# Kernel tuning notes

Hardware: AMD Instinct MI355X
Metric: run time of the kernel (lower is better)

The kernel has to match this reference:

```python
import jax, jax.numpy as jnp
import numpy as np

N_NODES = 100000
NEG_SLOPE = 0.2


def glorot(key, shape):
    fan_in, fan_out = shape[0], shape[-1]
    lim = jnp.sqrt(6.0 / (fan_in + fan_out))
    return jax.random.uniform(key, shape, jnp.float32, -lim, lim)


def setup_inputs() -> dict:
    key = jax.random.key(0)
    ks = jax.random.split(key, 16)
    x = jax.random.normal(ks[0], (N_NODES, 128), jnp.float32)
    edge_index = jax.random.randint(ks[1], (2, 1600000), 0, N_NODES, jnp.int64)
    H1, C1 = 4, 32
    C2 = 64
    return {
        "x": x,
        "edge_index": edge_index,
        # layer 1: GATv2Conv(128 -> 32, heads=4, concat)
        "Wl1": glorot(ks[2], (128, H1 * C1)), "bl1": jnp.zeros((H1 * C1,), jnp.float32),
        "Wr1": glorot(ks[3], (128, H1 * C1)), "br1": jnp.zeros((H1 * C1,), jnp.float32),
        "att1": glorot(ks[4], (H1, C1)),
        "bias1": jnp.zeros((H1 * C1,), jnp.float32),
        # layer 2: GATv2Conv(128 -> 64, heads=1, concat)
        "Wl2": glorot(ks[5], (H1 * C1, C2)), "bl2": jnp.zeros((C2,), jnp.float32),
        "Wr2": glorot(ks[6], (H1 * C1, C2)), "br2": jnp.zeros((C2,), jnp.float32),
        "att2": glorot(ks[7], (1, C2)),
        "bias2": jnp.zeros((C2,), jnp.float32),
    }


def gatv2_layer(x, src, dst, Wl, bl, Wr, br, att, bias):
    # x: [N, F_in]; src/dst: [E] (self-loops already appended)
    H, C = att.shape
    n = x.shape[0]
    xl = (x @ Wl + bl).reshape(n, H, C)  # source transform
    xr = (x @ Wr + br).reshape(n, H, C)  # target transform
    e = jax.nn.leaky_relu(xl[src] + xr[dst], NEG_SLOPE)          # [E, H, C]
    score = jnp.einsum('ehc,hc->eh', e, att)                     # [E, H]
    # segment softmax over incoming edges of each destination node
    smax = jax.ops.segment_max(score, dst, num_segments=n)       # [N, H]
    ex = jnp.exp(score - smax[dst])
    denom = jax.ops.segment_sum(ex, dst, num_segments=n)
    alpha = ex / denom[dst]                                      # [E, H]
    out = jax.ops.segment_sum(alpha[:, :, None] * xl[src], dst, num_segments=n)
    return out.reshape(n, H * C) + bias


def reference(x, edge_index, Wl1, bl1, Wr1, br1, att1, bias1,
              Wl2, bl2, Wr2, br2, att2, bias2):
    n = x.shape[0]
    loops = jnp.arange(n, dtype=edge_index.dtype)
    src = jnp.concatenate([edge_index[0], loops])
    dst = jnp.concatenate([edge_index[1], loops])
    h = gatv2_layer(x, src, dst, Wl1, bl1, Wr1, br1, att1, bias1)
    h = jax.nn.relu(h)
    out = gatv2_layer(h, src, dst, Wl2, bl2, Wr2, br2, att2, bias2)
    return out
```

## Files before the change

### kernel.cpp

```cpp
#include <hip/hip_runtime.h>
#include <hip/hip_fp16.h>

#define NEG 0.2f

typedef _Float16 f16x8 __attribute__((ext_vector_type(8)));
typedef _Float16 f16x2 __attribute__((ext_vector_type(2)));
typedef float    f32x4 __attribute__((ext_vector_type(4)));

__device__ __forceinline__ float fdot2h(__half2 a, __half2 b, float c) {
    return __builtin_amdgcn_fdot2(__builtin_bit_cast(f16x2, a),
                                  __builtin_bit_cast(f16x2, b), c, false);
}

__device__ __forceinline__ __half2 u2h2(unsigned int u) {
    return __builtin_bit_cast(__half2, u);
}

__device__ __forceinline__ __half2 hmax2(__half2 a, __half2 b) {
    unsigned int ua = __builtin_bit_cast(unsigned int, a);
    unsigned int ub = __builtin_bit_cast(unsigned int, b);
    unsigned int ud;
    asm("v_pk_max_f16 %0, %1, %2" : "=v"(ud) : "v"(ua), "v"(ub));
    return __builtin_bit_cast(__half2, ud);
}

template<int CTRL>
__device__ __forceinline__ float dppadd(float x) {
    int xi = __builtin_bit_cast(int, x);
    int yi = __builtin_amdgcn_update_dpp(0, xi, CTRL, 0xf, 0xf, true);
    return x + __builtin_bit_cast(float, yi);
}

template<int CPW, bool IN_F16, bool HPL>
__global__ __launch_bounds__(256) void mfma_gemm_k(
    const float* __restrict__ Xf, const __half* __restrict__ Xh,
    const float* __restrict__ Wl, const float* __restrict__ bl,
    const float* __restrict__ Wr, const float* __restrict__ br,
    __half* __restrict__ YL, __half* __restrict__ YR, int nrows)
{
    __shared__ _Float16 Xs[128 * 136];
    __shared__ _Float16 Ws[128 * 136];

    const int t    = threadIdx.x;
    const int row0 = blockIdx.x * 128;
    const int c0   = blockIdx.y * 128;

    if constexpr (IN_F16) {
        for (int i = t; i < 128 * 16; i += 256) {
            int r = i >> 4, c = i & 15;
            int gr = row0 + r;
            uint4 v = make_uint4(0u, 0u, 0u, 0u);
            if (gr < nrows) v = ((const uint4*)Xh)[(long)gr * 16 + c];
            *(uint4*)&Xs[r * 136 + c * 8] = v;
        }
    } else {
        for (int i = t; i < 128 * 16; i += 256) {
            int r = i >> 4, c = i & 15;
            int gr = row0 + r;
            float4 a = make_float4(0.f,0.f,0.f,0.f), b4 = make_float4(0.f,0.f,0.f,0.f);
            if (gr < nrows) {
                a  = ((const float4*)Xf)[(long)gr * 32 + c * 2];
                b4 = ((const float4*)Xf)[(long)gr * 32 + c * 2 + 1];
            }
            _Float16 h[8] = {(_Float16)a.x,(_Float16)a.y,(_Float16)a.z,(_Float16)a.w,
                             (_Float16)b4.x,(_Float16)b4.y,(_Float16)b4.z,(_Float16)b4.w};
            *(f16x8*)&Xs[r * 136 + c * 8] = *(f16x8*)h;
        }
    }

    for (int i = t; i < 128 * 128; i += 256) {
        int k = i >> 7, n = i & 127;
        int gc = c0 + n;
        const float* Wp = (gc >= CPW) ? Wr : Wl;
        int lc = gc & (CPW - 1);
        Ws[n * 136 + k] = (_Float16)Wp[(long)k * CPW + lc];
    }
    __syncthreads();

    const int lane  = t & 63;
    const int wv    = t >> 6;
    const int m     = lane & 15;
    const int quad  = lane >> 4;
    const int rbase = wv * 32;

    f16x8 Af[2][4];
    #pragma unroll
    for (int rt = 0; rt < 2; ++rt)
        #pragma unroll
        for (int ks = 0; ks < 4; ++ks)
            Af[rt][ks] = *(const f16x8*)&Xs[(rbase + rt * 16 + m) * 136 + ks * 32 + quad * 8];

    f32x4 acc[2][8];
    #pragma unroll
    for (int rt = 0; rt < 2; ++rt)
        #pragma unroll
        for (int ct = 0; ct < 8; ++ct)
            acc[rt][ct] = (f32x4){0.f, 0.f, 0.f, 0.f};

    #pragma unroll
    for (int ct = 0; ct < 8; ++ct) {
        #pragma unroll
        for (int ks = 0; ks < 4; ++ks) {
            f16x8 Bf = *(const f16x8*)&Ws[(ct * 16 + m) * 136 + ks * 32 + quad * 8];
            acc[0][ct] = __builtin_amdgcn_mfma_f32_16x16x32_f16(Af[0][ks], Bf, acc[0][ct], 0, 0, 0);
            acc[1][ct] = __builtin_amdgcn_mfma_f32_16x16x32_f16(Af[1][ks], Bf, acc[1][ct], 0, 0, 0);
        }
    }

    #pragma unroll
    for (int ct = 0; ct < 8; ++ct) {
        int gc = c0 + ct * 16 + m;
        int which = gc / CPW;
        int lc = gc % CPW;
        _Float16* Y = (_Float16*)(which ? YR : YL);
        float bv = (which ? br : bl)[lc];
        #pragma unroll
        for (int rt = 0; rt < 2; ++rt) {
            int rr = row0 + rbase + rt * 16 + quad * 4;
            #pragma unroll
            for (int g = 0; g < 4; ++g) {
                int r = rr + g;
                if (r < nrows) {
                    long idx;
                    if (HPL && which == 0)
                        idx = (long)(lc >> 6) * ((long)nrows * 64) + (long)r * 64 + (lc & 63);
                    else
                        idx = (long)r * CPW + lc;
                    Y[idx] = (_Float16)(acc[rt][ct][g] + bv);
                }
            }
        }
    }
}


__global__ __launch_bounds__(256) void h1_k(
    const int* __restrict__ ei, int* __restrict__ gh, int E0, int ET, int NBK)
{
    __shared__ int h[256];
    const int t = threadIdx.x, blk = blockIdx.x;
    h[t] = 0;
    __syncthreads();
    int e = blk * 4096 + t;
    #pragma unroll
    for (int u = 0; u < 16; ++u, e += 256) {
        if (e < ET) {
            int dst = (e < E0) ? ei[E0 + e] : (e - E0);
            atomicAdd(&h[dst >> 9], 1);
        }
    }
    __syncthreads();
    gh[t * NBK + blk] = h[t];
}

__global__ __launch_bounds__(256) void scan1_k(
    const int* __restrict__ cnt, int* __restrict__ loc, int* __restrict__ bsum, int n)
{
    __shared__ int wsum[4];
    int t = threadIdx.x;
    int i0 = blockIdx.x * 1024 + t * 4;
    int4 v;
    v.x = (i0 + 0 < n) ? cnt[i0 + 0] : 0;
    v.y = (i0 + 1 < n) ? cnt[i0 + 1] : 0;
    v.z = (i0 + 2 < n) ? cnt[i0 + 2] : 0;
    v.w = (i0 + 3 < n) ? cnt[i0 + 3] : 0;
    int tsum = v.x + v.y + v.z + v.w;
    int incl = tsum;
    #pragma unroll
    for (int s = 1; s < 64; s <<= 1) {
        int u = __shfl_up(incl, s, 64);
        if ((t & 63) >= s) incl += u;
    }
    int wid = t >> 6;
    if ((t & 63) == 63) wsum[wid] = incl;
    __syncthreads();
    int woff = 0;
    #pragma unroll
    for (int w = 0; w < 4; ++w) if (w < wid) woff += wsum[w];
    int ex = woff + incl - tsum;
    if (i0 + 0 < n) loc[i0 + 0] = ex;
    if (i0 + 1 < n) loc[i0 + 1] = ex + v.x;
    if (i0 + 2 < n) loc[i0 + 2] = ex + v.x + v.y;
    if (i0 + 3 < n) loc[i0 + 3] = ex + v.x + v.y + v.z;
    if (t == 255) bsum[blockIdx.x] = woff + incl;
}

__global__ void scan2_k(const int* __restrict__ bsum, int* __restrict__ bcarry,
                        int M, int* __restrict__ total_out)
{
    int lane = threadIdx.x;
    int carry = 0;
    for (int base = 0; base < M; base += 64) {
        int i = base + lane;
        int v = (i < M) ? bsum[i] : 0;
        int incl = v;
        #pragma unroll
        for (int s = 1; s < 64; s <<= 1) {
            int u = __shfl_up(incl, s, 64);
            if (lane >= s) incl += u;
        }
        if (i < M) bcarry[i] = carry + incl - v;
        carry += __shfl(incl, 63, 64);
    }
    if (lane == 0) *total_out = carry;
}

__global__ __launch_bounds__(256) void scan3_k(
    int* __restrict__ off, const int* __restrict__ bcarry, int n)
{
    int i = blockIdx.x * 256 + threadIdx.x;
    if (i >= n) return;
    off[i] += bcarry[i >> 10];
}

__global__ __launch_bounds__(256) void sc1_k(
    const int* __restrict__ ei, const int* __restrict__ gh,
    uint2* __restrict__ rec, int E0, int ET, int NBK)
{
    __shared__ int lofs[256];
    const int t = threadIdx.x, blk = blockIdx.x;
    lofs[t] = gh[t * NBK + blk];
    __syncthreads();
    int e = blk * 4096 + t;
    #pragma unroll
    for (int u = 0; u < 16; ++u, e += 256) {
        if (e < ET) {
            int src = (e < E0) ? ei[e]      : (e - E0);
            int dst = (e < E0) ? ei[E0 + e] : (e - E0);
            int p = atomicAdd(&lofs[dst >> 9], 1);
            rec[p] = make_uint2((unsigned)src, (unsigned)dst);
        }
    }
}

__global__ __launch_bounds__(256) void p2_k(
    const uint2* __restrict__ rec, const int* __restrict__ gh,
    int* __restrict__ srcs, int* __restrict__ off, int N, int NBK)
{
    __shared__ int hist[512];
    __shared__ int sc[2][512];
    __shared__ int curo[512];
    const int t = threadIdx.x;
    const int b = blockIdx.x;
    const int base = gh[b * NBK];
    const int end  = gh[(b + 1) * NBK];
    hist[t] = 0; hist[t + 256] = 0;
    __syncthreads();
    for (int i = base + t; i < end; i += 256) {
        uint2 r = rec[i];
        atomicAdd(&hist[r.y & 511], 1);
    }
    __syncthreads();
    sc[0][t] = hist[t]; sc[0][t + 256] = hist[t + 256];
    __syncthreads();
    int pp = 0;
    for (int s = 1; s < 512; s <<= 1, pp ^= 1) {
        int j0 = t, j1 = t + 256;
        sc[pp ^ 1][j0] = sc[pp][j0] + ((j0 >= s) ? sc[pp][j0 - s] : 0);
        sc[pp ^ 1][j1] = sc[pp][j1] + ((j1 >= s) ? sc[pp][j1 - s] : 0);
        __syncthreads();
    }
    {
        int j0 = t, j1 = t + 256;
        int e0 = base + sc[pp][j0] - hist[j0];
        int e1 = base + sc[pp][j1] - hist[j1];
        curo[j0] = e0;
        curo[j1] = e1;
        int d0 = b * 512 + j0, d1 = b * 512 + j1;
        if (d0 < N) off[d0] = e0;
        if (d1 < N) off[d1] = e1;
    }
    __syncthreads();
    for (int i = base + t; i < end; i += 256) {
        uint2 r = rec[i];
        int pos = atomicAdd(&curo[r.y & 511], 1);
        srcs[pos] = (int)r.x;
    }
}

template<bool RELU>
__global__ __launch_bounds__(256) void fused128hp_k(
    const __half* __restrict__ XLp, const __half* __restrict__ XR,
    const float* __restrict__ ATT, const int* __restrict__ srcs,
    const int* __restrict__ off, const float* __restrict__ bias,
    __half* __restrict__ OUT, int N, int p)
{
    const int t   = threadIdx.x;
    const int d   = blockIdx.x * 32 + (t >> 3);
    const int sub = t & 7;
    const bool nv = d < N;

    int a = 0, b = 0;
    if (nv) { a = off[d]; b = off[d + 1]; }

    __half2 xr[4] = { u2h2(0), u2h2(0), u2h2(0), u2h2(0) };
    if (nv) {
        uint4 ur = *(const uint4*)(XR + (long)d * 128 + p * 64 + sub * 8);
        xr[0] = u2h2(ur.x); xr[1] = u2h2(ur.y); xr[2] = u2h2(ur.z); xr[3] = u2h2(ur.w);
    }
    float4 at0f = ((const float4*)ATT)[p * 16 + sub * 2];
    float4 at1f = ((const float4*)ATT)[p * 16 + sub * 2 + 1];
    __half2 at[4] = { __floats2half2_rn(at0f.x, at0f.y), __floats2half2_rn(at0f.z, at0f.w),
                      __floats2half2_rn(at1f.x, at1f.y), __floats2half2_rn(at1f.z, at1f.w) };
    const __half2 neg2 = __float2half2_rn(NEG);

    float l = 0.f;
    float accv[8] = {0.f,0.f,0.f,0.f,0.f,0.f,0.f,0.f};

    const uint4* XL4 = (const uint4*)(XLp + (size_t)p * N * 64);

    if (b > a) {
        const int bm1 = b - 1;
        int sA = srcs[a];
        uint4 r0 = XL4[(long)sA * 8 + sub];
        int i1 = (a + 1 < bm1) ? a + 1 : bm1;
        int sB = srcs[i1];
        uint4 r1 = XL4[(long)sB * 8 + sub];
        int i2 = (a + 2 < bm1) ? a + 2 : bm1;
        int s2 = srcs[i2];

        for (int e = a; e < b; ++e) {
            uint4 r2 = XL4[(long)s2 * 8 + sub];
            int i3 = (e + 3 < bm1) ? e + 3 : bm1;
            int s3 = srcs[i3];

            __half2 x0 = u2h2(r0.x), x1 = u2h2(r0.y), x2 = u2h2(r0.z), x3 = u2h2(r0.w);
            __half2 s0h = __hadd2(x0, xr[0]);
            __half2 s1h = __hadd2(x1, xr[1]);
            __half2 s2h = __hadd2(x2, xr[2]);
            __half2 s3h = __hadd2(x3, xr[3]);
            __half2 q0 = hmax2(s0h, __hmul2(s0h, neg2));
            __half2 q1 = hmax2(s1h, __hmul2(s1h, neg2));
            __half2 q2 = hmax2(s2h, __hmul2(s2h, neg2));
            __half2 q3 = hmax2(s3h, __hmul2(s3h, neg2));
            float p0 = fdot2h(q0, at[0], 0.f);
            p0 = fdot2h(q1, at[1], p0);
            p0 = fdot2h(q2, at[2], p0);
            p0 = fdot2h(q3, at[3], p0);
            p0 = dppadd<0xB1>(p0);
            p0 = dppadd<0x4E>(p0);
            float ex = __expf(p0);
            l += ex;
            float2 f0 = __half22float2(x0), f1 = __half22float2(x1);
            float2 f2 = __half22float2(x2), f3 = __half22float2(x3);
            accv[0] += ex * f0.x; accv[1] += ex * f0.y;
            accv[2] += ex * f1.x; accv[3] += ex * f1.y;
            accv[4] += ex * f2.x; accv[5] += ex * f2.y;
            accv[6] += ex * f3.x; accv[7] += ex * f3.y;

            r0 = r1; r1 = r2; s2 = s3;
        }
    }

    if (nv) {
        float inv = 1.f / l;
        float4 b0 = ((const float4*)bias)[p * 16 + sub * 2];
        float4 b1 = ((const float4*)bias)[p * 16 + sub * 2 + 1];
        float o[8] = { accv[0]*inv + b0.x, accv[1]*inv + b0.y,
                       accv[2]*inv + b0.z, accv[3]*inv + b0.w,
                       accv[4]*inv + b1.x, accv[5]*inv + b1.y,
                       accv[6]*inv + b1.z, accv[7]*inv + b1.w };
        if constexpr (RELU) {
            #pragma unroll
            for (int j = 0; j < 8; ++j) o[j] = fmaxf(o[j], 0.f);
        }
        uint4 uo;
        uo.x = __builtin_bit_cast(unsigned int, __floats2half2_rn(o[0], o[1]));
        uo.y = __builtin_bit_cast(unsigned int, __floats2half2_rn(o[2], o[3]));
        uo.z = __builtin_bit_cast(unsigned int, __floats2half2_rn(o[4], o[5]));
        uo.w = __builtin_bit_cast(unsigned int, __floats2half2_rn(o[6], o[7]));
        *(uint4*)(OUT + (long)d * 128 + p * 64 + sub * 8) = uo;
    }
}

template<bool RELU>
__global__ __launch_bounds__(256) void fused64_k(
    const __half* __restrict__ XL, const __half* __restrict__ XR,
    const float* __restrict__ ATT, const int* __restrict__ srcs,
    const int* __restrict__ off, const float* __restrict__ bias,
    float* __restrict__ OUT, int N)
{
    const int t   = threadIdx.x;
    const int d   = blockIdx.x * 32 + (t >> 3);
    const int sub = t & 7;
    const bool nv = d < N;

    int a = 0, b = 0;
    if (nv) { a = off[d]; b = off[d + 1]; }

    __half2 xr[4] = { u2h2(0), u2h2(0), u2h2(0), u2h2(0) };
    if (nv) {
        uint4 ur = *(const uint4*)(XR + (long)d * 64 + sub * 8);
        xr[0] = u2h2(ur.x); xr[1] = u2h2(ur.y); xr[2] = u2h2(ur.z); xr[3] = u2h2(ur.w);
    }
    float4 at0f = ((const float4*)ATT)[sub * 2];
    float4 at1f = ((const float4*)ATT)[sub * 2 + 1];
    __half2 at[4] = { __floats2half2_rn(at0f.x, at0f.y), __floats2half2_rn(at0f.z, at0f.w),
                      __floats2half2_rn(at1f.x, at1f.y), __floats2half2_rn(at1f.z, at1f.w) };
    const __half2 neg2 = __float2half2_rn(NEG);

    float l = 0.f;
    float accv[8] = {0.f,0.f,0.f,0.f,0.f,0.f,0.f,0.f};

    const uint4* XL4 = (const uint4*)XL;

    if (b > a) {
        const int bm1 = b - 1;
        int sA = srcs[a];
        uint4 r0 = XL4[(long)sA * 8 + sub];
        int i1 = (a + 1 < bm1) ? a + 1 : bm1;
        int sB = srcs[i1];
        uint4 r1 = XL4[(long)sB * 8 + sub];
        int i2 = (a + 2 < bm1) ? a + 2 : bm1;
        int s2 = srcs[i2];

        for (int e = a; e < b; ++e) {
            uint4 r2 = XL4[(long)s2 * 8 + sub];
            int i3 = (e + 3 < bm1) ? e + 3 : bm1;
            int s3 = srcs[i3];

            __half2 x0 = u2h2(r0.x), x1 = u2h2(r0.y), x2 = u2h2(r0.z), x3 = u2h2(r0.w);
            __half2 s0h = __hadd2(x0, xr[0]);
            __half2 s1h = __hadd2(x1, xr[1]);
            __half2 s2h = __hadd2(x2, xr[2]);
            __half2 s3h = __hadd2(x3, xr[3]);
            __half2 q0 = hmax2(s0h, __hmul2(s0h, neg2));
            __half2 q1 = hmax2(s1h, __hmul2(s1h, neg2));
            __half2 q2 = hmax2(s2h, __hmul2(s2h, neg2));
            __half2 q3 = hmax2(s3h, __hmul2(s3h, neg2));
            float p0 = fdot2h(q0, at[0], 0.f);
            p0 = fdot2h(q1, at[1], p0);
            p0 = fdot2h(q2, at[2], p0);
            p0 = fdot2h(q3, at[3], p0);
            p0 = dppadd<0xB1>(p0);
            p0 = dppadd<0x4E>(p0);
            p0 = dppadd<0x141>(p0);
            float ex = __expf(p0);
            l += ex;
            float2 f0 = __half22float2(x0), f1 = __half22float2(x1);
            float2 f2 = __half22float2(x2), f3 = __half22float2(x3);
            accv[0] += ex * f0.x; accv[1] += ex * f0.y;
            accv[2] += ex * f1.x; accv[3] += ex * f1.y;
            accv[4] += ex * f2.x; accv[5] += ex * f2.y;
            accv[6] += ex * f3.x; accv[7] += ex * f3.y;

            r0 = r1; r1 = r2; s2 = s3;
        }
    }

    if (nv) {
        float inv = 1.f / l;
        float4 b0 = ((const float4*)bias)[sub * 2];
        float4 b1 = ((const float4*)bias)[sub * 2 + 1];
        float4 o0 = make_float4(accv[0]*inv + b0.x, accv[1]*inv + b0.y,
                                accv[2]*inv + b0.z, accv[3]*inv + b0.w);
        float4 o1 = make_float4(accv[4]*inv + b1.x, accv[5]*inv + b1.y,
                                accv[6]*inv + b1.z, accv[7]*inv + b1.w);
        if constexpr (RELU) {
            o0.x = fmaxf(o0.x, 0.f); o0.y = fmaxf(o0.y, 0.f);
            o0.z = fmaxf(o0.z, 0.f); o0.w = fmaxf(o0.w, 0.f);
            o1.x = fmaxf(o1.x, 0.f); o1.y = fmaxf(o1.y, 0.f);
            o1.z = fmaxf(o1.z, 0.f); o1.w = fmaxf(o1.w, 0.f);
        }
        *(float4*)(OUT + (long)d * 64 + sub * 8)     = o0;
        *(float4*)(OUT + (long)d * 64 + sub * 8 + 4) = o1;
    }
}

extern "C" void kernel_launch(void* const* d_in, const int* in_sizes, int n_in,
                              void* d_out, int out_size, void* d_ws, size_t ws_size,
                              hipStream_t stream)
{
    const float* x     = (const float*)d_in[0];
    const int*   ei    = (const int*)  d_in[1];
    const float* Wl1   = (const float*)d_in[2];
    const float* bl1   = (const float*)d_in[3];
    const float* Wr1   = (const float*)d_in[4];
    const float* br1   = (const float*)d_in[5];
    const float* att1  = (const float*)d_in[6];
    const float* bias1 = (const float*)d_in[7];
    const float* Wl2   = (const float*)d_in[8];
    const float* bl2   = (const float*)d_in[9];
    const float* Wr2   = (const float*)d_in[10];
    const float* br2   = (const float*)d_in[11];
    const float* att2  = (const float*)d_in[12];
    const float* bias2 = (const float*)d_in[13];

    const int  N  = in_sizes[0] / 128;
    const int  E0 = in_sizes[1] / 2;
    const int  ET = E0 + N;

    char* w = (char*)d_ws;
    __half* XLh = (__half*)w;
    __half* XRh = XLh + (size_t)N * 128;
    __half* Cch = XRh + (size_t)N * 128;
    int*    off = (int*)(Cch + (size_t)N * 128);
    int*    srcs= off + (N + 1);
    int*    gh  = srcs + ET;
    uint2*  rec = (uint2*)w;
    float*  out = (float*)d_out;

    dim3 b256(256);
    const int gx    = (N + 127) / 128;
    const int ng32  = (N + 31) / 32;

    const int NBK   = (ET + 4095) / 4096;
    const int n1    = 256 * NBK;
    const int NB1   = (n1 + 1023) / 1024;
    const int NBUCK = (N + 511) / 512;
    int* bsum = gh + n1;
    int* bcar = bsum + NB1;

    h1_k<<<NBK, b256, 0, stream>>>(ei, gh, E0, ET, NBK);
    scan1_k<<<NB1, b256, 0, stream>>>(gh, gh, bsum, n1);
    scan2_k<<<1, 64, 0, stream>>>(bsum, bcar, NB1, off + N);
    scan3_k<<<(n1 + 255) / 256, b256, 0, stream>>>(gh, bcar, n1);
    sc1_k<<<NBK, b256, 0, stream>>>(ei, gh, rec, E0, ET, NBK);
    p2_k<<<NBUCK, b256, 0, stream>>>(rec, gh, srcs, off, N, NBK);

    mfma_gemm_k<128, false, true><<<dim3(gx, 2), b256, 0, stream>>>(
        x, nullptr, Wl1, bl1, Wr1, br1, XLh, XRh, N);
    fused128hp_k<true><<<ng32, b256, 0, stream>>>(XLh, XRh, att1, srcs, off, bias1, Cch, N, 0);
    fused128hp_k<true><<<ng32, b256, 0, stream>>>(XLh, XRh, att1, srcs, off, bias1, Cch, N, 1);

    mfma_gemm_k<64, true, false><<<dim3(gx, 1), b256, 0, stream>>>(
        nullptr, Cch, Wl2, bl2, Wr2, br2, XLh, XRh, N);
    fused64_k<false><<<ng32, b256, 0, stream>>>(XLh, XRh, att2, srcs, off, bias2, out, N);
}
```

Measured before the change: 406.8 us.

## Replace tiled GEMM with persistent per-wave transform kernel loading weights once

The node-feature GEMMs become a persistent kernel. Each block converts the full weight matrix (both Wl and Wr, all output columns) to fp16 in shared memory once. Each wave then loops over 16-row tiles, loading A fragments straight from global memory and prefetching the next tile into registers. This removes the repeated per-block weight staging, the X staging through shared memory, and the duplicated X reads across column blocks. In exchange each block needs a larger shared-memory footprint (COLS*136 halfs), and each tile gets less MFMA work to hide global load latency behind.

```diff
diff --git a/kernel.cpp b/kernel.cpp
--- a/kernel.cpp
+++ b/kernel.cpp
@@ -31,108 +31,103 @@
     return x + __builtin_bit_cast(float, yi);
 }
 
-template<int CPW, bool IN_F16, bool HPL>
-__global__ __launch_bounds__(256) void mfma_gemm_k(
+template<int COLS, bool IN_F16, bool HPL>
+__global__ __launch_bounds__(256) void xform_k(
     const float* __restrict__ Xf, const __half* __restrict__ Xh,
     const float* __restrict__ Wl, const float* __restrict__ bl,
     const float* __restrict__ Wr, const float* __restrict__ br,
     __half* __restrict__ YL, __half* __restrict__ YR, int nrows)
 {
-    __shared__ _Float16 Xs[128 * 136];
-    __shared__ _Float16 Ws[128 * 136];
-
-    const int t    = threadIdx.x;
-    const int row0 = blockIdx.x * 128;
-    const int c0   = blockIdx.y * 128;
-
-    if constexpr (IN_F16) {
-        for (int i = t; i < 128 * 16; i += 256) {
-            int r = i >> 4, c = i & 15;
-            int gr = row0 + r;
-            uint4 v = make_uint4(0u, 0u, 0u, 0u);
-            if (gr < nrows) v = ((const uint4*)Xh)[(long)gr * 16 + c];
-            *(uint4*)&Xs[r * 136 + c * 8] = v;
-        }
-    } else {
-        for (int i = t; i < 128 * 16; i += 256) {
-            int r = i >> 4, c = i & 15;
-            int gr = row0 + r;
-            float4 a = make_float4(0.f,0.f,0.f,0.f), b4 = make_float4(0.f,0.f,0.f,0.f);
-            if (gr < nrows) {
-                a  = ((const float4*)Xf)[(long)gr * 32 + c * 2];
-                b4 = ((const float4*)Xf)[(long)gr * 32 + c * 2 + 1];
+    constexpr int CPW = COLS / 2;
+    __shared__ _Float16 Ws[COLS * 136];
+
+    const int t = threadIdx.x;
+    for (int i = t; i < 128 * COLS; i += 256) {
+        int k = i / COLS, c = i % COLS;
+        const float* Wp = (c >= CPW) ? Wr : Wl;
+        int lc = c - ((c >= CPW) ? CPW : 0);
+        Ws[c * 136 + k] = (_Float16)Wp[(long)k * CPW + lc];
+    }
+    __syncthreads();
+
+    const int lane = t & 63, wv = t >> 6;
+    const int m = lane & 15, quad = lane >> 4;
+
+    float bv[COLS / 16];
+    #pragma unroll
+    for (int ct = 0; ct < COLS / 16; ++ct) {
+        int col = ct * 16 + m;
+        bv[ct] = (col >= CPW) ? br[col - CPW] : bl[col];
+    }
+
+    const int ntiles = (nrows + 15) >> 4;
+    const int stride = gridDim.x * 4;
+
+    int tile = blockIdx.x * 4 + wv;
+    if (tile >= ntiles) return;
+
+    f16x8 A0[4], A1[4];
+
+    auto loadA = [&](int tl, f16x8* Af) {
+        int row = tl * 16 + m;
+        if (row >= nrows) row = nrows - 1;
+        if constexpr (IN_F16) {
+            const uint4* Xp = (const uint4*)(Xh + (long)row * 128);
+            #pragma unroll
+            for (int ks = 0; ks < 4; ++ks) {
+                uint4 v = Xp[ks * 4 + quad];
+                Af[ks] = __builtin_bit_cast(f16x8, v);
             }
-            _Float16 h[8] = {(_Float16)a.x,(_Float16)a.y,(_Float16)a.z,(_Float16)a.w,
-                             (_Float16)b4.x,(_Float16)b4.y,(_Float16)b4.z,(_Float16)b4.w};
-            *(f16x8*)&Xs[r * 136 + c * 8] = *(f16x8*)h;
-        }
-    }
-
-    for (int i = t; i < 128 * 128; i += 256) {
-        int k = i >> 7, n = i & 127;
-        int gc = c0 + n;
-        const float* Wp = (gc >= CPW) ? Wr : Wl;
-        int lc = gc & (CPW - 1);
-        Ws[n * 136 + k] = (_Float16)Wp[(long)k * CPW + lc];
-    }
-    __syncthreads();
-
-    const int lane  = t & 63;
-    const int wv    = t >> 6;
-    const int m     = lane & 15;
-    const int quad  = lane >> 4;
-    const int rbase = wv * 32;
-
-    f16x8 Af[2][4];
-    #pragma unroll
-    for (int rt = 0; rt < 2; ++rt)
+        } else {
+            const float4* Xp = (const float4*)(Xf + (long)row * 128);
+            #pragma unroll
+            for (int ks = 0; ks < 4; ++ks) {
+                float4 a = Xp[ks * 8 + quad * 2];
+                float4 b = Xp[ks * 8 + quad * 2 + 1];
+                _Float16 h[8] = {(_Float16)a.x,(_Float16)a.y,(_Float16)a.z,(_Float16)a.w,
+                                 (_Float16)b.x,(_Float16)b.y,(_Float16)b.z,(_Float16)b.w};
+                Af[ks] = *(f16x8*)h;
+            }
+        }
+    };
+
+    loadA(tile, A0);
+
+    for (; tile < ntiles; tile += stride) {
+        int nt = tile + stride;
+        if (nt < ntiles) loadA(nt, A1);
+
+        const int row0 = tile * 16;
         #pragma unroll
-        for (int ks = 0; ks < 4; ++ks)
-            Af[rt][ks] = *(const f16x8*)&Xs[(rbase + rt * 16 + m) * 136 + ks * 32 + quad * 8];
-
-    f32x4 acc[2][8];
-    #pragma unroll
-    for (int rt = 0; rt < 2; ++rt)
-        #pragma unroll
-        for (int ct = 0; ct < 8; ++ct)
-            acc[rt][ct] = (f32x4){0.f, 0.f, 0.f, 0.f};
-
-    #pragma unroll
-    for (int ct = 0; ct < 8; ++ct) {
-        #pragma unroll
-        for (int ks = 0; ks < 4; ++ks) {
-            f16x8 Bf = *(const f16x8*)&Ws[(ct * 16 + m) * 136 + ks * 32 + quad * 8];
-            acc[0][ct] = __builtin_amdgcn_mfma_f32_16x16x32_f16(Af[0][ks], Bf, acc[0][ct], 0, 0, 0);
-            acc[1][ct] = __builtin_amdgcn_mfma_f32_16x16x32_f16(Af[1][ks], Bf, acc[1][ct], 0, 0, 0);
-        }
-    }
-
-    #pragma unroll
-    for (int ct = 0; ct < 8; ++ct) {
-        int gc = c0 + ct * 16 + m;
-        int which = gc / CPW;
-        int lc = gc % CPW;
-        _Float16* Y = (_Float16*)(which ? YR : YL);
-        float bv = (which ? br : bl)[lc];
-        #pragma unroll
-        for (int rt = 0; rt < 2; ++rt) {
-            int rr = row0 + rbase + rt * 16 + quad * 4;
+        for (int ct = 0; ct < COLS / 16; ++ct) {
+            f32x4 acc = (f32x4){0.f, 0.f, 0.f, 0.f};
+            #pragma unroll
+            for (int ks = 0; ks < 4; ++ks) {
+                f16x8 Bf = *(const f16x8*)&Ws[(ct * 16 + m) * 136 + ks * 32 + quad * 8];
+                acc = __builtin_amdgcn_mfma_f32_16x16x32_f16(A0[ks], Bf, acc, 0, 0, 0);
+            }
+            int col = ct * 16 + m;
+            int which = col >= CPW;
+            int lc = col - (which ? CPW : 0);
+            _Float16* Y = (_Float16*)(which ? YR : YL);
+            int rb = row0 + quad * 4;
             #pragma unroll
             for (int g = 0; g < 4; ++g) {
-                int r = rr + g;
+                int r = rb + g;
                 if (r < nrows) {
                     long idx;
-                    if (HPL && which == 0)
+                    if (HPL && !which)
                         idx = (long)(lc >> 6) * ((long)nrows * 64) + (long)r * 64 + (lc & 63);
                     else
                         idx = (long)r * CPW + lc;
-                    Y[idx] = (_Float16)(acc[rt][ct][g] + bv);
+                    Y[idx] = (_Float16)(acc[g] + bv[ct]);
                 }
             }
         }
-    }
-}
-
+        #pragma unroll
+        for (int ks = 0; ks < 4; ++ks) A0[ks] = A1[ks];
+    }
+}
 
 __global__ __launch_bounds__(256) void h1_k(
     const int* __restrict__ ei, int* __restrict__ gh, int E0, int ET, int NBK)
@@ -501,7 +496,6 @@
     float*  out = (float*)d_out;
 
     dim3 b256(256);
-    const int gx    = (N + 127) / 128;
     const int ng32  = (N + 31) / 32;
 
     const int NBK   = (ET + 4095) / 4096;
@@ -518,12 +512,12 @@
     sc1_k<<<NBK, b256, 0, stream>>>(ei, gh, rec, E0, ET, NBK);
     p2_k<<<NBUCK, b256, 0, stream>>>(rec, gh, srcs, off, N, NBK);
 
-    mfma_gemm_k<128, false, true><<<dim3(gx, 2), b256, 0, stream>>>(
+    xform_k<256, false, true><<<512, b256, 0, stream>>>(
         x, nullptr, Wl1, bl1, Wr1, br1, XLh, XRh, N);
     fused128hp_k<true><<<ng32, b256, 0, stream>>>(XLh, XRh, att1, srcs, off, bias1, Cch, N, 0);
     fused128hp_k<true><<<ng32, b256, 0, stream>>>(XLh, XRh, att1, srcs, off, bias1, Cch, N, 1);
 
-    mfma_gemm_k<64, true, false><<<dim3(gx, 1), b256, 0, stream>>>(
+    xform_k<128, true, false><<<1024, b256, 0, stream>>>(
         nullptr, Cch, Wl2, bl2, Wr2, br2, XLh, XRh, N);
     fused64_k<false><<<ng32, b256, 0, stream>>>(XLh, XRh, att2, srcs, off, bias2, out, N);
 }
```

Result: faster. 367.9 us (-9.6%).
